# Performance work log

Hardware: AMD Instinct MI355X
Metric: run time of the kernel (lower is better)

The kernel has to match this reference:

```python
import jax, jax.numpy as jnp
import numpy as np

B, S, D, H, HD = 1, 4096, 512, 8, 64
FF = 2048
ROT = 32          # rotary dim (RotaryEmbedding(dim=32))
THETA = 10000.0
EPS = 1e-5


def setup_inputs() -> dict:
    key = jax.random.key(0)
    ks = jax.random.split(key, 10)
    s = 0.02
    return {
        "x": jax.random.normal(ks[0], (B, S, D), jnp.float32),
        "gammas": jnp.ones((2,), jnp.float32),
        "betas": jnp.zeros((2,), jnp.float32),
        "wq": jax.random.normal(ks[1], (D, D), jnp.float32) * s,
        "wk": jax.random.normal(ks[2], (D, D), jnp.float32) * s,
        "wv": jax.random.normal(ks[3], (D, D), jnp.float32) * s,
        "wo": jax.random.normal(ks[4], (D, D), jnp.float32) * s,
        "bo": jnp.zeros((D,), jnp.float32),
        "w1": jax.random.normal(ks[5], (D, FF), jnp.float32) * s,
        "b1": jnp.zeros((FF,), jnp.float32),
        "w2": jax.random.normal(ks[6], (FF, D), jnp.float32) * s,
        "b2": jnp.zeros((D,), jnp.float32),
        "mask": jax.random.randint(ks[7], (B, 1, 1, S), 0, 2, jnp.int32),
    }


def _ln(x):  # LayerNorm, no affine (elementwise_affine=False)
    m = x.mean(-1, keepdims=True)
    v = ((x - m) ** 2).mean(-1, keepdims=True)
    return (x - m) / jnp.sqrt(v + EPS)


def _rope_tables(seq_len, dtype):
    inv_freq = 1.0 / (THETA ** (jnp.arange(0, ROT, 2, dtype=jnp.float32) / ROT))
    freqs = jnp.arange(seq_len, dtype=jnp.float32)[:, None] * inv_freq[None, :]  # (S, ROT/2)
    freqs = jnp.repeat(freqs, 2, axis=-1)  # interleaved: f0,f0,f1,f1,... (S, ROT)
    return jnp.cos(freqs).astype(dtype), jnp.sin(freqs).astype(dtype)


def _apply_rope(t, cos, sin):
    # t: (B,H,S,HD); rotate first ROT dims with interleaved pairs (lucidrains)
    tr, tp = t[..., :ROT], t[..., ROT:]
    x1, x2 = tr[..., 0::2], tr[..., 1::2]
    rot = jnp.stack((-x2, x1), axis=-1).reshape(tr.shape)
    return jnp.concatenate([tr * cos + rot * sin, tp], axis=-1)


def reference(x, gammas, betas, wq, wk, wv, wo, bo, w1, b1, w2, b2, mask):
    # --- attention block ---
    res = x
    h = _ln(x)
    h = gammas[0] * h + betas[0]  # FiLM
    q = (h @ wq).reshape(B, S, H, HD).transpose(0, 2, 1, 3)
    k = (h @ wk).reshape(B, S, H, HD).transpose(0, 2, 1, 3)
    v = (h @ wv).reshape(B, S, H, HD).transpose(0, 2, 1, 3)
    cos, sin = _rope_tables(S, x.dtype)
    q = _apply_rope(q, cos, sin)
    k = _apply_rope(k, cos, sin)
    score = jnp.einsum("bhqd,bhkd->bhqk", q, k) / jnp.sqrt(jnp.asarray(HD, x.dtype))
    score = jnp.where(mask == 0, jnp.asarray(-1e9, x.dtype), score)
    attn = jax.nn.softmax(score, axis=-1)
    out = jnp.einsum("bhqk,bhkd->bhqd", attn, v)
    out = out.transpose(0, 2, 1, 3).reshape(B, S, D)
    x = res + (out @ wo + bo)
    # --- FFN block ---
    res = x
    h = _ln(x)
    h = gammas[1] * h + betas[1]
    h = jax.nn.gelu(h @ w1 + b1, approximate=False) @ w2 + b2
    return res + h
```

## Files before the change

kernel.cpp:

```cpp
#include <hip/hip_runtime.h>
#include <math.h>

constexpr int SEQ  = 4096;
constexpr int DIM  = 512;
constexpr int NH   = 8;
constexpr int HDIM = 64;
constexpr int FFD  = 2048;
constexpr int KSPLIT = 3;

typedef unsigned short u16;
typedef __attribute__((ext_vector_type(8))) short bf16x8;
typedef __attribute__((ext_vector_type(4))) float f32x4;
typedef __attribute__((ext_vector_type(8))) unsigned short u16x8;

#define LOG2E      1.4426950408889634f
#define QSCALE     (0.125f * LOG2E)
#define MASK_ON    (-8.0f * LOG2E)
#define MASK_OFF   (-1.4427e9f)

static __device__ __forceinline__ u16 f2bf(float x) {
    union { float f; unsigned int u; } v; v.f = x;
    unsigned int r = v.u + 0x7fff + ((v.u >> 16) & 1);
    return (u16)(r >> 16);
}
static __device__ __forceinline__ float bf2f(u16 h) {
    union { unsigned int u; float f; } v; v.u = ((unsigned int)h) << 16;
    return v.f;
}
static __device__ __forceinline__ unsigned int cvtpk(float lo, float hi) {
    unsigned int r;
    asm volatile("v_cvt_pk_bf16_f32 %0, %1, %2" : "=v"(r) : "v"(lo), "v"(hi));
    return r;
}
static __device__ __forceinline__ float exp2f_fast(float x) {
    float r; asm volatile("v_exp_f32 %0, %1" : "=v"(r) : "v"(x)); return r;
}
static __device__ __forceinline__ void gload_lds16(const void* g, void* l) {
    __builtin_amdgcn_global_load_lds(
        (const __attribute__((address_space(1))) unsigned int*)g,
        (__attribute__((address_space(3))) unsigned int*)l, 16, 0, 0);
}

__global__ void prep_kernel(const float* __restrict__ x, u16* __restrict__ h1,
                            const float* __restrict__ gammas, const float* __restrict__ betas,
                            const float* __restrict__ wq, const float* __restrict__ wk,
                            const float* __restrict__ wv, const float* __restrict__ wo,
                            const float* __restrict__ w1, const float* __restrict__ w2,
                            u16* __restrict__ wqkvT, u16* __restrict__ woT,
                            u16* __restrict__ w1T, u16* __restrict__ w2T,
                            const int* __restrict__ mask, float* __restrict__ maskc,
                            int* __restrict__ kidx, int* __restrict__ nkp,
                            float* __restrict__ ct, float* __restrict__ st) {
    __shared__ float smem[1056];
    int b = blockIdx.x;
    int t = threadIdx.x;
    if (b < SEQ) {
        const float* xr = x + (size_t)b * DIM;
        float v0 = xr[t], v1 = xr[t + 256];
        float* rs = smem; float* rq = smem + 256;
        rs[t] = v0 + v1;
        rq[t] = v0 * v0 + v1 * v1;
        __syncthreads();
        for (int o = 128; o > 0; o >>= 1) {
            if (t < o) { rs[t] += rs[t + o]; rq[t] += rq[t + o]; }
            __syncthreads();
        }
        float mean = rs[0] / DIM;
        float var  = rq[0] / DIM - mean * mean;
        float rstd = rsqrtf(var + 1e-5f);
        float g = gammas[0], be = betas[0];
        h1[(size_t)b * DIM + t]       = f2bf(g * ((v0 - mean) * rstd) + be);
        h1[(size_t)b * DIM + t + 256] = f2bf(g * ((v1 - mean) * rstd) + be);
        return;
    }
    b -= SEQ;
    if (b == 0 && blockIdx.x == SEQ) { }
    if (b < 1) {
        __shared__ int cnt[256];
        int base = t * 16;
        int loc[16]; int c = 0;
#pragma unroll
        for (int i = 0; i < 16; i++) { loc[i] = mask[base + i]; c += (loc[i] != 0); }
        cnt[t] = c;
        __syncthreads();
        for (int o = 1; o < 256; o <<= 1) {
            int v = (t >= o) ? cnt[t - o] : 0;
            __syncthreads();
            cnt[t] += v;
            __syncthreads();
        }
        int pos = cnt[t] - c;
        int total = cnt[255];
#pragma unroll
        for (int i = 0; i < 16; i++)
            if (loc[i]) kidx[pos++] = base + i;
#pragma unroll
        for (int i = 0; i < 16; i++)
            maskc[base + i] = (base + i < total) ? MASK_ON : MASK_OFF;
        if (t == 0) *nkp = total;
        return;
    }
    b -= 1;
    if (b < 256) {
        int idx = b * 256 + t;
        int s = idx >> 4, i = idx & 15;
        float invf = expf(-(float)i * (9.2103403719761836f / 16.0f));
        float freq = (float)s * invf;
        ct[idx] = cosf(freq);
        st[idx] = sinf(freq);
        return;
    }
    b -= 256;
    const float* src; u16* dst; int K, N; float scale = 1.f;
    if (b < 256)       { src = wq; dst = wqkvT;            K = 512;  N = 512; scale = QSCALE; }
    else if (b < 512)  { src = wk; dst = wqkvT + 512*512;  K = 512;  N = 512; b -= 256; }
    else if (b < 768)  { src = wv; dst = wqkvT + 1024*512; K = 512;  N = 512; b -= 512; }
    else if (b < 1024) { src = wo; dst = woT;              K = 512;  N = 512; b -= 768; }
    else if (b < 2048) { src = w1; dst = w1T;              K = 512;  N = 2048; b -= 1024; }
    else               { src = w2; dst = w2T;              K = 2048; N = 512;  b -= 2048; }
    float (*tile)[33] = (float(*)[33])smem;
    int tiles_x = N / 32;
    int n0 = (b % tiles_x) * 32, k0 = (b / tiles_x) * 32;
    int tx = t & 31, ty = t >> 5;
#pragma unroll
    for (int i = 0; i < 4; i++) {
        int kk = ty + i * 8;
        tile[kk][tx] = src[(size_t)(k0 + kk) * N + n0 + tx];
    }
    __syncthreads();
#pragma unroll
    for (int i = 0; i < 4; i++) {
        int nn = ty + i * 8;
        dst[(size_t)(n0 + nn) * K + k0 + tx] = f2bf(scale * tile[tx][nn]);
    }
}

__global__ void ln_bf16_kernel(const u16* __restrict__ x, u16* __restrict__ out,
                               const float* __restrict__ gammas, const float* __restrict__ betas,
                               int gi) {
    int row = blockIdx.x;
    int t = threadIdx.x;
    unsigned int u = *(const unsigned int*)(x + (size_t)row * DIM + t * 2);
    float v0 = bf2f((u16)(u & 0xffff)), v1 = bf2f((u16)(u >> 16));
    __shared__ float rs[256], rq[256];
    rs[t] = v0 + v1;
    rq[t] = v0 * v0 + v1 * v1;
    __syncthreads();
    for (int o = 128; o > 0; o >>= 1) {
        if (t < o) { rs[t] += rs[t + o]; rq[t] += rq[t + o]; }
        __syncthreads();
    }
    float mean = rs[0] / DIM;
    float var  = rq[0] / DIM - mean * mean;
    float rstd = rsqrtf(var + 1e-5f);
    float g = gammas[gi], b = betas[gi];
    *(unsigned int*)(out + (size_t)row * DIM + t * 2) =
        cvtpk(g * ((v0 - mean) * rstd) + b, g * ((v1 - mean) * rstd) + b);
}

constexpr int FLAG_BF16 = 1, FLAG_GELU = 2, FLAG_SPLIT = 4, FLAG_ROPE = 8, FLAG_RESID_BF16 = 16;

template<int MF>
__global__ __launch_bounds__(256) void gemm_bf16(
    const u16* __restrict__ A, const u16* __restrict__ WT,
    const float* __restrict__ bias, const void* __restrict__ resid,
    void* __restrict__ Cq, int M, int N, int K, int flags)
{
    constexpr int BM = MF * 64;
    __shared__ __align__(16) u16 At[2][BM * 128];
    __shared__ __align__(16) u16 Bt[2][64 * 128];
    const int t = threadIdx.x, lane = t & 63, w = t >> 6;
    const int n0 = blockIdx.x * 64, m0 = blockIdx.y * BM;
    const int l15 = lane & 15, l4 = lane >> 4;

    f32x4 acc[MF][4];
#pragma unroll
    for (int m = 0; m < MF; m++)
#pragma unroll
        for (int n = 0; n < 4; n++) acc[m][n] = (f32x4){0.f, 0.f, 0.f, 0.f};

    auto stage = [&](int buf, int k0) {
#pragma unroll
        for (int i = 0; i < MF * 4; i++) {
            int c = (w * MF * 4 + i) * 64 + lane;
            int r = c >> 4, jj = (c & 15) ^ (r & 7);
            gload_lds16(A + (size_t)(m0 + r) * K + k0 + jj * 8,
                        (char*)At[buf] + (w * MF * 4 + i) * 1024);
        }
#pragma unroll
        for (int i = 0; i < 4; i++) {
            int c = (w * 4 + i) * 64 + lane;
            int r = c >> 4, jj = (c & 15) ^ (r & 7);
            gload_lds16(WT + (size_t)(n0 + r) * K + k0 + jj * 8,
                        (char*)Bt[buf] + (w * 4 + i) * 1024);
        }
    };

    const int NT = K / 128;
    stage(0, 0);
    for (int ti = 0; ti < NT; ti++) {
        const int cur = ti & 1;
        asm volatile("s_waitcnt vmcnt(0)" ::: "memory");
        __syncthreads();
        if (ti + 1 < NT) stage(cur ^ 1, (ti + 1) * 128);
        __builtin_amdgcn_s_setprio(1);
#pragma unroll
        for (int kk = 0; kk < 4; kk++) {
            bf16x8 af[MF], bfr[4];
#pragma unroll
            for (int m = 0; m < MF; m++) {
                int row = w * MF * 16 + m * 16 + l15;
                af[m] = *(bf16x8*)((char*)At[cur] + row * 256 +
                                   ((kk * 64 + l4 * 16) ^ ((row & 7) << 4)));
            }
#pragma unroll
            for (int n = 0; n < 4; n++) {
                int row = n * 16 + l15;
                bfr[n] = *(bf16x8*)((char*)Bt[cur] + row * 256 +
                                    ((kk * 64 + l4 * 16) ^ ((row & 7) << 4)));
            }
#pragma unroll
            for (int m = 0; m < MF; m++)
#pragma unroll
                for (int n = 0; n < 4; n++)
                    acc[m][n] = __builtin_amdgcn_mfma_f32_16x16x32_bf16(
                        af[m], bfr[n], acc[m][n], 0, 0, 0);
        }
        __builtin_amdgcn_s_setprio(0);
    }

#pragma unroll
    for (int m = 0; m < MF; m++)
#pragma unroll
        for (int rr = 0; rr < 4; rr++) {
            int row = m0 + w * MF * 16 + m * 16 + l4 * 4 + rr;
#pragma unroll
            for (int n = 0; n < 4; n++) {
                int colg = n0 + n * 16 + l15;
                float cv = acc[m][n][rr];
                if (bias) cv += bias[colg];
                if (flags & FLAG_GELU) cv = 0.5f * cv * (1.0f + erff(cv * 0.70710678118f));
                if (resid) {
                    if (flags & FLAG_RESID_BF16)
                        cv += bf2f(((const u16*)resid)[(size_t)row * N + colg]);
                    else
                        cv += ((const float*)resid)[(size_t)row * N + colg];
                }
                if (flags & FLAG_BF16) {
                    ((u16*)Cq)[(size_t)row * N + colg] = f2bf(cv);
                } else {
                    ((float*)Cq)[(size_t)row * N + colg] = cv;
                }
            }
        }
}

__global__ __launch_bounds__(256) void gemm128(
    const u16* __restrict__ A, const u16* __restrict__ WT,
    const float* __restrict__ bias,
    void* __restrict__ Cq, void* __restrict__ Ck, void* __restrict__ Cv,
    const float* __restrict__ ct, const float* __restrict__ st,
    int M, int N, int K, int flags)
{
    __shared__ __align__(16) u16 At[2][128 * 64];
    __shared__ __align__(16) u16 Bt[2][128 * 64];
    const int t = threadIdx.x, lane = t & 63, w = t >> 6;
    const int wm = w >> 1, wn = w & 1;
    const int n0 = blockIdx.x * 128, m0 = blockIdx.y * 128;
    const int l15 = lane & 15, l4 = lane >> 4;

    f32x4 acc[4][4];
#pragma unroll
    for (int m = 0; m < 4; m++)
#pragma unroll
        for (int n = 0; n < 4; n++) acc[m][n] = (f32x4){0.f, 0.f, 0.f, 0.f};

    auto stage = [&](int buf, int k0) {
#pragma unroll
        for (int i = 0; i < 4; i++) {
            int c = (w * 4 + i) * 64 + lane;
            int r = c >> 3, j = (c & 7) ^ (r & 7);
            gload_lds16(A + (size_t)(m0 + r) * K + k0 + j * 8,
                        (char*)At[buf] + (w * 4 + i) * 1024);
            gload_lds16(WT + (size_t)(n0 + r) * K + k0 + j * 8,
                        (char*)Bt[buf] + (w * 4 + i) * 1024);
        }
    };

    const int NT = K / 64;
    stage(0, 0);
    for (int ti = 0; ti < NT; ti++) {
        const int cur = ti & 1;
        asm volatile("s_waitcnt vmcnt(0)" ::: "memory");
        __syncthreads();
        if (ti + 1 < NT) stage(cur ^ 1, (ti + 1) * 64);
        __builtin_amdgcn_s_setprio(1);
#pragma unroll
        for (int kk = 0; kk < 2; kk++) {
            bf16x8 af[4], bfr[4];
#pragma unroll
            for (int m = 0; m < 4; m++) {
                int row = wm * 64 + m * 16 + l15;
                af[m] = *(bf16x8*)((char*)At[cur] + row * 128 +
                                   ((kk * 64 + l4 * 16) ^ ((row & 7) << 4)));
            }
#pragma unroll
            for (int n = 0; n < 4; n++) {
                int row = wn * 64 + n * 16 + l15;
                bfr[n] = *(bf16x8*)((char*)Bt[cur] + row * 128 +
                                    ((kk * 64 + l4 * 16) ^ ((row & 7) << 4)));
            }
#pragma unroll
            for (int m = 0; m < 4; m++)
#pragma unroll
                for (int n = 0; n < 4; n++)
                    acc[m][n] = __builtin_amdgcn_mfma_f32_16x16x32_bf16(
                        af[m], bfr[n], acc[m][n], 0, 0, 0);
        }
        __builtin_amdgcn_s_setprio(0);
    }

#pragma unroll
    for (int m = 0; m < 4; m++)
#pragma unroll
        for (int rr = 0; rr < 4; rr++) {
            int row = m0 + wm * 64 + m * 16 + l4 * 4 + rr;
#pragma unroll
            for (int n = 0; n < 4; n++) {
                int colg = n0 + wn * 64 + n * 16 + l15;
                float cv = acc[m][n][rr];
                if (bias) cv += bias[colg];
                int which = colg >> 9;
                if ((flags & FLAG_ROPE) && which < 2 && n < 2) {
                    float partner = __shfl_xor(cv, 1, 64);
                    int i = (n * 16 + l15) >> 1;
                    float cc = ct[row * 16 + i], ss = st[row * 16 + i];
                    cv = (l15 & 1) ? (cv * cc + partner * ss) : (cv * cc - partner * ss);
                }
                if (flags & FLAG_GELU) cv = 0.5f * cv * (1.0f + erff(cv * 0.70710678118f));
                if (flags & FLAG_SPLIT) {
                    u16* dst = which == 0 ? (u16*)Cq : which == 1 ? (u16*)Ck : (u16*)Cv;
                    dst[(size_t)row * 512 + (colg & 511)] = f2bf(cv);
                } else {
                    ((u16*)Cq)[(size_t)row * N + colg] = f2bf(cv);
                }
            }
        }
}

__global__ void gather_kt(const u16* __restrict__ k, const u16* __restrict__ v,
                          const int* __restrict__ kidx, const int* __restrict__ nkp,
                          u16* __restrict__ kc, u16* __restrict__ vTc) {
    __shared__ __align__(16) u16 tile[64][80];
    int h = blockIdx.y;
    int s0 = blockIdx.x * 64;
    int t = threadIdx.x;
    int nk = *nkp;
#pragma unroll
    for (int p = 0; p < 2; p++) {
        int c = p * 256 + t;
        int r = c >> 3, j = c & 7;
        int src = (s0 + r < nk) ? kidx[s0 + r] : -1;
        u16x8 kv = {}, vv = {};
        if (src >= 0) {
            kv = *(const u16x8*)(k + (size_t)src * DIM + h * HDIM + j * 8);
            vv = *(const u16x8*)(v + (size_t)src * DIM + h * HDIM + j * 8);
        }
        *(u16x8*)(kc + (size_t)(s0 + r) * DIM + h * HDIM + j * 8) = kv;
        *(u16x8*)&tile[r][j * 8] = vv;
    }
    __syncthreads();
#pragma unroll
    for (int p = 0; p < 2; p++) {
        int c = p * 256 + t;
        int d = c >> 3, j = c & 7;
        u16x8 vv;
#pragma unroll
        for (int i = 0; i < 8; i++) vv[i] = tile[j * 8 + i][d];
        *(u16x8*)(vTc + ((size_t)h * HDIM + d) * SEQ + s0 + j * 8) = vv;
    }
}

__global__ __launch_bounds__(256, 3) void fattn_kernel(
    const u16* __restrict__ q, const u16* __restrict__ k,
    const u16* __restrict__ vT, const float* __restrict__ maskc,
    const int* __restrict__ nkp,
    u16* __restrict__ Opart, float* __restrict__ lpart)
{
    __shared__ __align__(16) u16 k_s[2][64 * 64];
    __shared__ __align__(16) u16 vt_s[2][64 * 64];
    __shared__ __align__(16) u16 p_s[4][32 * 64];

    const int t = threadIdx.x;
    const int lane = t & 63;
    const int w = t >> 6;
    const int h = blockIdx.x;
    const int q0 = blockIdx.y * 128;
    const int split = blockIdx.z;
    const int nk = *nkp;
    const int ntiles = (nk + 63) >> 6;
    const int tstart = (split * ntiles) / 3;
    const int tend   = ((split + 1) * ntiles) / 3;
    const int l15 = lane & 15, g = lane >> 4;

    bf16x8 qf[2][2];
#pragma unroll
    for (int qh = 0; qh < 2; qh++) {
        const u16* qrow = q + (size_t)(q0 + w * 32 + qh * 16 + l15) * DIM + h * HDIM;
        qf[qh][0] = *(const bf16x8*)(qrow + g * 8);
        qf[qh][1] = *(const bf16x8*)(qrow + g * 8 + 32);
    }

    const bf16x8 ones = (bf16x8){16256, 16256, 16256, 16256, 16256, 16256, 16256, 16256};

    f32x4 O[2][4];
    f32x4 lacc[2];
#pragma unroll
    for (int qh = 0; qh < 2; qh++) {
#pragma unroll
        for (int dt = 0; dt < 4; dt++) O[qh][dt] = (f32x4){0.f, 0.f, 0.f, 0.f};
        lacc[qh] = (f32x4){0.f, 0.f, 0.f, 0.f};
    }

    char* pbase = (char*)p_s[w];
    const int psw = (l15 & 7) << 4;

    auto stage = [&](int buf, int kb2) {
#pragma unroll
        for (int i = 0; i < 2; i++) {
            int c = (w * 2 + i) * 64 + lane;
            int r = c >> 3, j = (c & 7) ^ (r & 7);
            gload_lds16(k + (size_t)(kb2 + r) * DIM + h * HDIM + j * 8,
                        (char*)k_s + buf * 8192 + (w * 2 + i) * 1024);
            gload_lds16(vT + ((size_t)h * HDIM + r) * SEQ + kb2 + j * 8,
                        (char*)vt_s + buf * 8192 + (w * 2 + i) * 1024);
        }
    };

    if (tstart < tend) stage(0, tstart * 64);
    for (int ti = tstart; ti < tend; ti++) {
        const int cur = (ti - tstart) & 1;
        const int kb = ti * 64;
        asm volatile("s_waitcnt vmcnt(0)" ::: "memory");
        __syncthreads();
        if (ti + 1 < tend) stage(cur ^ 1, kb + 64);

        char* kcur = (char*)k_s + cur * 8192;
        char* vcur = (char*)vt_s + cur * 8192;

        f32x4 sacc[2][4];
        __builtin_amdgcn_s_setprio(1);
#pragma unroll
        for (int kt = 0; kt < 4; kt++) {
            int key = kt * 16 + l15;
            int ksw = (key & 7) << 4;
            char* kbase = kcur + key * 128;
            bf16x8 a0 = *(bf16x8*)(kbase + ((g * 16)      ^ ksw));
            bf16x8 a1 = *(bf16x8*)(kbase + ((g * 16 + 64) ^ ksw));
#pragma unroll
            for (int qh = 0; qh < 2; qh++) {
                f32x4 z = (f32x4){0.f, 0.f, 0.f, 0.f};
                z = __builtin_amdgcn_mfma_f32_16x16x32_bf16(a0, qf[qh][0], z, 0, 0, 0);
                z = __builtin_amdgcn_mfma_f32_16x16x32_bf16(a1, qf[qh][1], z, 0, 0, 0);
                sacc[qh][kt] = z;
            }
        }
        __builtin_amdgcn_s_setprio(0);

        float4 mf4[4];
#pragma unroll
        for (int kt = 0; kt < 4; kt++)
            mf4[kt] = *(const float4*)(maskc + kb + kt * 16 + g * 4);
#pragma unroll
        for (int qh = 0; qh < 2; qh++)
#pragma unroll
            for (int kt = 0; kt < 4; kt++) {
                float p0 = exp2f_fast(sacc[qh][kt][0] + mf4[kt].x);
                float p1 = exp2f_fast(sacc[qh][kt][1] + mf4[kt].y);
                float p2 = exp2f_fast(sacc[qh][kt][2] + mf4[kt].z);
                float p3 = exp2f_fast(sacc[qh][kt][3] + mf4[kt].w);
                uint2 pk;
                pk.x = cvtpk(p0, p1);
                pk.y = cvtpk(p2, p3);
                int colb = (kt * 16 + g * 4) * 2;
                *(uint2*)(pbase + (qh * 16 + l15) * 128 + (colb ^ psw)) = pk;
            }

        __builtin_amdgcn_s_setprio(1);
#pragma unroll
        for (int h2 = 0; h2 < 2; h2++) {
            bf16x8 pb[2];
#pragma unroll
            for (int qh = 0; qh < 2; qh++)
                pb[qh] = *(bf16x8*)(pbase + (qh * 16 + l15) * 128 +
                                    (((h2 * 4 + g) * 16) ^ psw));
#pragma unroll
            for (int dt = 0; dt < 4; dt++) {
                int d = dt * 16 + l15;
                bf16x8 va = *(bf16x8*)(vcur + d * 128 +
                                       (((h2 * 4 + g) * 16) ^ ((d & 7) << 4)));
#pragma unroll
                for (int qh = 0; qh < 2; qh++)
                    O[qh][dt] = __builtin_amdgcn_mfma_f32_16x16x32_bf16(
                        va, pb[qh], O[qh][dt], 0, 0, 0);
            }
#pragma unroll
            for (int qh = 0; qh < 2; qh++)
                lacc[qh] = __builtin_amdgcn_mfma_f32_16x16x32_bf16(
                    ones, pb[qh], lacc[qh], 0, 0, 0);
        }
        __builtin_amdgcn_s_setprio(0);
    }

#pragma unroll
    for (int qh = 0; qh < 2; qh++) {
        float lrun = lacc[qh][0];
        int row = q0 + w * 32 + qh * 16 + l15;
        u16* orow = Opart + (size_t)split * SEQ * DIM + (size_t)row * DIM + h * HDIM;
#pragma unroll
        for (int dt = 0; dt < 4; dt++)
#pragma unroll
            for (int r = 0; r < 4; r += 2) {
                unsigned int pk = cvtpk(O[qh][dt][r], O[qh][dt][r + 1]);
                *(unsigned int*)(orow + dt * 16 + 4 * g + r) = pk;
            }
        if (g == 0)
            lpart[((size_t)split * NH + h) * SEQ + row] = lrun;
    }
}

__global__ void attn_combine(const u16* __restrict__ Opart, const float* __restrict__ lpart,
                             u16* __restrict__ out) {
    int t = threadIdx.x;
    int row = blockIdx.x * 4 + (t >> 6);
    int col = (t & 63) * 8;
    int h = col >> 6;
    float l = lpart[(size_t)h * SEQ + row]
            + lpart[((size_t)NH + h) * SEQ + row]
            + lpart[((size_t)2 * NH + h) * SEQ + row];
    float inv = 1.0f / l;
    const size_t SD = (size_t)SEQ * DIM;
    const u16* base = Opart + (size_t)row * DIM + col;
    u16x8 ua = *(const u16x8*)(base);
    u16x8 ub = *(const u16x8*)(base + SD);
    u16x8 uc = *(const u16x8*)(base + 2 * SD);
    u16x8 res;
#pragma unroll
    for (int j = 0; j < 8; j += 2) {
        float o0 = bf2f(ua[j])     + bf2f(ub[j])     + bf2f(uc[j]);
        float o1 = bf2f(ua[j + 1]) + bf2f(ub[j + 1]) + bf2f(uc[j + 1]);
        unsigned int pk = cvtpk(o0 * inv, o1 * inv);
        res[j]     = (u16)(pk & 0xffff);
        res[j + 1] = (u16)(pk >> 16);
    }
    *(u16x8*)(out + (size_t)row * DIM + col) = res;
}

extern "C" void kernel_launch(void* const* d_in, const int* in_sizes, int n_in,
                              void* d_out, int out_size, void* d_ws, size_t ws_size,
                              hipStream_t stream) {
    const float* x      = (const float*)d_in[0];
    const float* gammas = (const float*)d_in[1];
    const float* betas  = (const float*)d_in[2];
    const float* wq     = (const float*)d_in[3];
    const float* wk     = (const float*)d_in[4];
    const float* wv     = (const float*)d_in[5];
    const float* wo     = (const float*)d_in[6];
    const float* bo     = (const float*)d_in[7];
    const float* w1     = (const float*)d_in[8];
    const float* b1     = (const float*)d_in[9];
    const float* w2     = (const float*)d_in[10];
    const float* b2     = (const float*)d_in[11];
    const int*   mask   = (const int*)d_in[12];
    float* out = (float*)d_out;

    char* wsb = (char*)d_ws;
    u16*   h1b   = (u16*)(wsb + 0);
    u16*   kb    = (u16*)(wsb + (4ull  << 20));
    u16*   vb    = (u16*)(wsb + (8ull  << 20));
    u16*   vTc   = (u16*)(wsb + (12ull << 20));
    u16*   qb    = (u16*)(wsb + (16ull << 20));
    u16*   Opart = (u16*)(wsb + (20ull << 20));
    u16*   x2b   = (u16*)(wsb + (20ull << 20));
    u16*   wqkvT = (u16*)(wsb + (32ull << 20));
    u16*   woT   = wqkvT + 1536 * 512;
    u16*   w1T   = woT   + 512 * 512;
    u16*   w2T   = w1T   + 2048 * 512;
    float* maskc = (float*)(wsb + (38ull << 20));
    int*   kidx  = (int*)(wsb + (38ull << 20) + (64 << 10));
    int*   nkp   = (int*)(wsb + (38ull << 20) + (128 << 10));
    float* ct    = (float*)(wsb + (39ull << 20));
    float* st    = ct + 65536;
    float* lpart = (float*)vb;
    u16*   kc    = h1b;
    u16*   f1b   = h1b;
    u16*   h2b   = qb;
    u16*   attnb = h1b;

    prep_kernel<<<SEQ + 1 + 256 + 3072, 256, 0, stream>>>(
        x, h1b, gammas, betas, wq, wk, wv, wo, w1, w2,
        wqkvT, woT, w1T, w2T, mask, maskc, kidx, nkp, ct, st);
    gemm128<<<dim3(1536 / 128, SEQ / 128), 256, 0, stream>>>(
        h1b, wqkvT, nullptr, qb, kb, vb, ct, st,
        SEQ, 1536, DIM, FLAG_SPLIT | FLAG_BF16 | FLAG_ROPE);
    gather_kt<<<dim3(SEQ / 64, NH), 256, 0, stream>>>(kb, vb, kidx, nkp, kc, vTc);
    fattn_kernel<<<dim3(NH, SEQ / 128, KSPLIT), 256, 0, stream>>>(
        qb, kc, vTc, maskc, nkp, Opart, lpart);
    attn_combine<<<SEQ / 4, 256, 0, stream>>>(Opart, lpart, attnb);
    gemm_bf16<1><<<dim3(DIM / 64, SEQ / 64), 256, 0, stream>>>(
        attnb, woT, bo, (const void*)x, x2b, SEQ, DIM, DIM, FLAG_BF16);
    ln_bf16_kernel<<<SEQ, 256, 0, stream>>>(x2b, h2b, gammas, betas, 1);
    gemm128<<<dim3(FFD / 128, SEQ / 128), 256, 0, stream>>>(
        h2b, w1T, b1, f1b, nullptr, nullptr, nullptr, nullptr,
        SEQ, FFD, DIM, FLAG_BF16 | FLAG_GELU);
    gemm_bf16<1><<<dim3(DIM / 64, SEQ / 64), 256, 0, stream>>>(
        f1b, w2T, b2, (const void*)x2b, out, SEQ, DIM, FFD, FLAG_RESID_BF16);
}
```

Baseline: 159.7 us.

## Scatter compacted K/V in QKV GEMM epilogue and use wave-per-row LayerNorm

The QKV GEMM epilogue now uses an inverse index built from the mask to write K and V rows directly into compacted positions. Masked-out rows are skipped, so the separate gather kernel only has to transpose V and can exit early for blocks beyond the valid key count. Both LayerNorm paths switch from block-wide shared-memory tree reductions to one wavefront per row, with vectorized 8-element loads and shuffle reductions. The cost is a per-row index lookup in the epilogue. Compacted K rows past the valid count are no longer zeroed, so they hold stale workspace data and rely on the mask to be ignored.

```diff
diff --git a/kernel.cpp b/kernel.cpp
--- a/kernel.cpp
+++ b/kernel.cpp
@@ -49,32 +49,42 @@
                             u16* __restrict__ wqkvT, u16* __restrict__ woT,
                             u16* __restrict__ w1T, u16* __restrict__ w2T,
                             const int* __restrict__ mask, float* __restrict__ maskc,
-                            int* __restrict__ kidx, int* __restrict__ nkp,
+                            int* __restrict__ invidx, int* __restrict__ nkp,
                             float* __restrict__ ct, float* __restrict__ st) {
     __shared__ float smem[1056];
     int b = blockIdx.x;
     int t = threadIdx.x;
-    if (b < SEQ) {
-        const float* xr = x + (size_t)b * DIM;
-        float v0 = xr[t], v1 = xr[t + 256];
-        float* rs = smem; float* rq = smem + 256;
-        rs[t] = v0 + v1;
-        rq[t] = v0 * v0 + v1 * v1;
-        __syncthreads();
-        for (int o = 128; o > 0; o >>= 1) {
-            if (t < o) { rs[t] += rs[t + o]; rq[t] += rq[t + o]; }
-            __syncthreads();
-        }
-        float mean = rs[0] / DIM;
-        float var  = rq[0] / DIM - mean * mean;
+    if (b < SEQ / 4) {
+        int wv_ = t >> 6, lane = t & 63;
+        int row = b * 4 + wv_;
+        const float* xr = x + (size_t)row * DIM + lane * 8;
+        float4 a0 = *(const float4*)xr;
+        float4 a1 = *(const float4*)(xr + 4);
+        float f[8] = {a0.x, a0.y, a0.z, a0.w, a1.x, a1.y, a1.z, a1.w};
+        float s = 0.f, qs = 0.f;
+#pragma unroll
+        for (int i = 0; i < 8; i++) { s += f[i]; qs += f[i] * f[i]; }
+#pragma unroll
+        for (int o = 1; o < 64; o <<= 1) {
+            s  += __shfl_xor(s, o, 64);
+            qs += __shfl_xor(qs, o, 64);
+        }
+        float mean = s / DIM;
+        float var  = qs / DIM - mean * mean;
         float rstd = rsqrtf(var + 1e-5f);
         float g = gammas[0], be = betas[0];
-        h1[(size_t)b * DIM + t]       = f2bf(g * ((v0 - mean) * rstd) + be);
-        h1[(size_t)b * DIM + t + 256] = f2bf(g * ((v1 - mean) * rstd) + be);
+        u16x8 res;
+#pragma unroll
+        for (int i = 0; i < 8; i += 2) {
+            unsigned int pk = cvtpk(g * ((f[i] - mean) * rstd) + be,
+                                    g * ((f[i + 1] - mean) * rstd) + be);
+            res[i]     = (u16)(pk & 0xffff);
+            res[i + 1] = (u16)(pk >> 16);
+        }
+        *(u16x8*)(h1 + (size_t)row * DIM + lane * 8) = res;
         return;
     }
-    b -= SEQ;
-    if (b == 0 && blockIdx.x == SEQ) { }
+    b -= SEQ / 4;
     if (b < 1) {
         __shared__ int cnt[256];
         int base = t * 16;
@@ -93,7 +103,7 @@
         int total = cnt[255];
 #pragma unroll
         for (int i = 0; i < 16; i++)
-            if (loc[i]) kidx[pos++] = base + i;
+            invidx[base + i] = loc[i] ? pos++ : -1;
 #pragma unroll
         for (int i = 0; i < 16; i++)
             maskc[base + i] = (base + i < total) ? MASK_ON : MASK_OFF;
@@ -138,24 +148,32 @@
 __global__ void ln_bf16_kernel(const u16* __restrict__ x, u16* __restrict__ out,
                                const float* __restrict__ gammas, const float* __restrict__ betas,
                                int gi) {
-    int row = blockIdx.x;
     int t = threadIdx.x;
-    unsigned int u = *(const unsigned int*)(x + (size_t)row * DIM + t * 2);
-    float v0 = bf2f((u16)(u & 0xffff)), v1 = bf2f((u16)(u >> 16));
-    __shared__ float rs[256], rq[256];
-    rs[t] = v0 + v1;
-    rq[t] = v0 * v0 + v1 * v1;
-    __syncthreads();
-    for (int o = 128; o > 0; o >>= 1) {
-        if (t < o) { rs[t] += rs[t + o]; rq[t] += rq[t + o]; }
-        __syncthreads();
-    }
-    float mean = rs[0] / DIM;
-    float var  = rq[0] / DIM - mean * mean;
+    int wv_ = t >> 6, lane = t & 63;
+    int row = blockIdx.x * 4 + wv_;
+    u16x8 v = *(const u16x8*)(x + (size_t)row * DIM + lane * 8);
+    float f[8];
+    float s = 0.f, qs = 0.f;
+#pragma unroll
+    for (int i = 0; i < 8; i++) { f[i] = bf2f(v[i]); s += f[i]; qs += f[i] * f[i]; }
+#pragma unroll
+    for (int o = 1; o < 64; o <<= 1) {
+        s  += __shfl_xor(s, o, 64);
+        qs += __shfl_xor(qs, o, 64);
+    }
+    float mean = s / DIM;
+    float var  = qs / DIM - mean * mean;
     float rstd = rsqrtf(var + 1e-5f);
-    float g = gammas[gi], b = betas[gi];
-    *(unsigned int*)(out + (size_t)row * DIM + t * 2) =
-        cvtpk(g * ((v0 - mean) * rstd) + b, g * ((v1 - mean) * rstd) + b);
+    float g = gammas[gi], be = betas[gi];
+    u16x8 res;
+#pragma unroll
+    for (int i = 0; i < 8; i += 2) {
+        unsigned int pk = cvtpk(g * ((f[i] - mean) * rstd) + be,
+                                g * ((f[i + 1] - mean) * rstd) + be);
+        res[i]     = (u16)(pk & 0xffff);
+        res[i + 1] = (u16)(pk >> 16);
+    }
+    *(u16x8*)(out + (size_t)row * DIM + lane * 8) = res;
 }
 
 constexpr int FLAG_BF16 = 1, FLAG_GELU = 2, FLAG_SPLIT = 4, FLAG_ROPE = 8, FLAG_RESID_BF16 = 16;
@@ -260,6 +278,7 @@
     const float* __restrict__ bias,
     void* __restrict__ Cq, void* __restrict__ Ck, void* __restrict__ Cv,
     const float* __restrict__ ct, const float* __restrict__ st,
+    const int* __restrict__ invidx,
     int M, int N, int K, int flags)
 {
     __shared__ __align__(16) u16 At[2][128 * 64];
@@ -320,17 +339,19 @@
         __builtin_amdgcn_s_setprio(0);
     }
 
+    const int which = (n0 + wn * 64) >> 9;
 #pragma unroll
     for (int m = 0; m < 4; m++)
 #pragma unroll
         for (int rr = 0; rr < 4; rr++) {
             int row = m0 + wm * 64 + m * 16 + l4 * 4 + rr;
+            int orow = row;
+            if ((flags & FLAG_SPLIT) && which > 0) orow = invidx[row];
 #pragma unroll
             for (int n = 0; n < 4; n++) {
                 int colg = n0 + wn * 64 + n * 16 + l15;
                 float cv = acc[m][n][rr];
                 if (bias) cv += bias[colg];
-                int which = colg >> 9;
                 if ((flags & FLAG_ROPE) && which < 2 && n < 2) {
                     float partner = __shfl_xor(cv, 1, 64);
                     int i = (n * 16 + l15) >> 1;
@@ -339,8 +360,10 @@
                 }
                 if (flags & FLAG_GELU) cv = 0.5f * cv * (1.0f + erff(cv * 0.70710678118f));
                 if (flags & FLAG_SPLIT) {
-                    u16* dst = which == 0 ? (u16*)Cq : which == 1 ? (u16*)Ck : (u16*)Cv;
-                    dst[(size_t)row * 512 + (colg & 511)] = f2bf(cv);
+                    if (orow >= 0) {
+                        u16* dst = which == 0 ? (u16*)Cq : which == 1 ? (u16*)Ck : (u16*)Cv;
+                        dst[(size_t)orow * 512 + (colg & 511)] = f2bf(cv);
+                    }
                 } else {
                     ((u16*)Cq)[(size_t)row * N + colg] = f2bf(cv);
                 }
@@ -348,25 +371,21 @@
         }
 }
 
-__global__ void gather_kt(const u16* __restrict__ k, const u16* __restrict__ v,
-                          const int* __restrict__ kidx, const int* __restrict__ nkp,
-                          u16* __restrict__ kc, u16* __restrict__ vTc) {
+__global__ void transpose_c(const u16* __restrict__ vc, const int* __restrict__ nkp,
+                            u16* __restrict__ vTc) {
+    int nk = *nkp;
+    int s0 = blockIdx.x * 64;
+    if (s0 >= ((nk + 63) & ~63)) return;
     __shared__ __align__(16) u16 tile[64][80];
     int h = blockIdx.y;
-    int s0 = blockIdx.x * 64;
     int t = threadIdx.x;
-    int nk = *nkp;
 #pragma unroll
     for (int p = 0; p < 2; p++) {
         int c = p * 256 + t;
         int r = c >> 3, j = c & 7;
-        int src = (s0 + r < nk) ? kidx[s0 + r] : -1;
-        u16x8 kv = {}, vv = {};
-        if (src >= 0) {
-            kv = *(const u16x8*)(k + (size_t)src * DIM + h * HDIM + j * 8);
-            vv = *(const u16x8*)(v + (size_t)src * DIM + h * HDIM + j * 8);
-        }
-        *(u16x8*)(kc + (size_t)(s0 + r) * DIM + h * HDIM + j * 8) = kv;
+        u16x8 vv = {};
+        if (s0 + r < nk)
+            vv = *(const u16x8*)(vc + (size_t)(s0 + r) * DIM + h * HDIM + j * 8);
         *(u16x8*)&tile[r][j * 8] = vv;
     }
     __syncthreads();
@@ -576,8 +595,8 @@
 
     char* wsb = (char*)d_ws;
     u16*   h1b   = (u16*)(wsb + 0);
-    u16*   kb    = (u16*)(wsb + (4ull  << 20));
-    u16*   vb    = (u16*)(wsb + (8ull  << 20));
+    u16*   kc    = (u16*)(wsb + (4ull  << 20));
+    u16*   vc    = (u16*)(wsb + (8ull  << 20));
     u16*   vTc   = (u16*)(wsb + (12ull << 20));
     u16*   qb    = (u16*)(wsb + (16ull << 20));
     u16*   Opart = (u16*)(wsb + (20ull << 20));
@@ -587,31 +606,30 @@
     u16*   w1T   = woT   + 512 * 512;
     u16*   w2T   = w1T   + 2048 * 512;
     float* maskc = (float*)(wsb + (38ull << 20));
-    int*   kidx  = (int*)(wsb + (38ull << 20) + (64 << 10));
+    int*   invidx= (int*)(wsb + (38ull << 20) + (64 << 10));
     int*   nkp   = (int*)(wsb + (38ull << 20) + (128 << 10));
     float* ct    = (float*)(wsb + (39ull << 20));
     float* st    = ct + 65536;
-    float* lpart = (float*)vb;
-    u16*   kc    = h1b;
+    float* lpart = (float*)(wsb + (40ull << 20));
     u16*   f1b   = h1b;
     u16*   h2b   = qb;
     u16*   attnb = h1b;
 
-    prep_kernel<<<SEQ + 1 + 256 + 3072, 256, 0, stream>>>(
+    prep_kernel<<<SEQ / 4 + 1 + 256 + 3072, 256, 0, stream>>>(
         x, h1b, gammas, betas, wq, wk, wv, wo, w1, w2,
-        wqkvT, woT, w1T, w2T, mask, maskc, kidx, nkp, ct, st);
+        wqkvT, woT, w1T, w2T, mask, maskc, invidx, nkp, ct, st);
     gemm128<<<dim3(1536 / 128, SEQ / 128), 256, 0, stream>>>(
-        h1b, wqkvT, nullptr, qb, kb, vb, ct, st,
+        h1b, wqkvT, nullptr, qb, kc, vc, ct, st, invidx,
         SEQ, 1536, DIM, FLAG_SPLIT | FLAG_BF16 | FLAG_ROPE);
-    gather_kt<<<dim3(SEQ / 64, NH), 256, 0, stream>>>(kb, vb, kidx, nkp, kc, vTc);
+    transpose_c<<<dim3(SEQ / 64, NH), 256, 0, stream>>>(vc, nkp, vTc);
     fattn_kernel<<<dim3(NH, SEQ / 128, KSPLIT), 256, 0, stream>>>(
         qb, kc, vTc, maskc, nkp, Opart, lpart);
     attn_combine<<<SEQ / 4, 256, 0, stream>>>(Opart, lpart, attnb);
     gemm_bf16<1><<<dim3(DIM / 64, SEQ / 64), 256, 0, stream>>>(
         attnb, woT, bo, (const void*)x, x2b, SEQ, DIM, DIM, FLAG_BF16);
-    ln_bf16_kernel<<<SEQ, 256, 0, stream>>>(x2b, h2b, gammas, betas, 1);
+    ln_bf16_kernel<<<SEQ / 4, 256, 0, stream>>>(x2b, h2b, gammas, betas, 1);
     gemm128<<<dim3(FFD / 128, SEQ / 128), 256, 0, stream>>>(
-        h2b, w1T, b1, f1b, nullptr, nullptr, nullptr, nullptr,
+        h2b, w1T, b1, f1b, nullptr, nullptr, nullptr, nullptr, nullptr,
         SEQ, FFD, DIM, FLAG_BF16 | FLAG_GELU);
     gemm_bf16<1><<<dim3(DIM / 64, SEQ / 64), 256, 0, stream>>>(
         f1b, w2T, b2, (const void*)x2b, out, SEQ, DIM, FFD, FLAG_RESID_BF16);
```

Measured after the change: 151.4 us. 5.2% less time.
